# Kernel optimization log

Hardware: AMD Instinct MI355X
Metric: run time of the kernel (lower is better)

The kernel has to match this reference:

```python
import jax, jax.numpy as jnp
import numpy as np

NU = 500000   # num user nodes
NI = 100000   # num item nodes
F  = 300      # item feature dim
D  = 64       # hidden channels
E  = 2000000  # num rated edges
EL = 1000000  # num supervision (label) edges


def setup_inputs() -> dict:
    key = jax.random.key(0)
    ks = jax.random.split(key, 24)
    def nrm(k, shp, scale=0.05):
        return jax.random.normal(k, shp, dtype=jnp.float32) * scale
    inp = {
        "user_emb_w": nrm(ks[0], (NU, D)),
        "item_x": jax.random.normal(ks[1], (NI, F), dtype=jnp.float32),
        "item_lin_w": nrm(ks[2], (F, D)),
        "item_lin_b": jnp.zeros((D,), jnp.float32),
        "Wl1_ui": nrm(ks[3], (D, D)), "Wr1_ui": nrm(ks[4], (D, D)), "b1_ui": jnp.zeros((D,), jnp.float32),
        "Wl1_iu": nrm(ks[5], (D, D)), "Wr1_iu": nrm(ks[6], (D, D)), "b1_iu": jnp.zeros((D,), jnp.float32),
        "Wl2_ui": nrm(ks[7], (D, D)), "Wr2_ui": nrm(ks[8], (D, D)), "b2_ui": jnp.zeros((D,), jnp.float32),
        "Wl2_iu": nrm(ks[9], (D, D)), "Wr2_iu": nrm(ks[10], (D, D)), "b2_iu": jnp.zeros((D,), jnp.float32),
        "user_node_id": jnp.arange(NU, dtype=jnp.int32),
        "edge_src": jax.random.randint(ks[11], (E,), 0, NU, dtype=jnp.int32),
        "edge_dst": jax.random.randint(ks[12], (E,), 0, NI, dtype=jnp.int32),
        "label_src": jax.random.randint(ks[13], (EL,), 0, NU, dtype=jnp.int32),
        "label_dst": jax.random.randint(ks[14], (EL,), 0, NI, dtype=jnp.int32),
    }
    return inp


def _seg_mean(x_src, src, dst, n_dst):
    # mean-aggregate source features onto destination nodes (PyG SAGEConv aggr='mean')
    s = jax.ops.segment_sum(x_src[src], dst, num_segments=n_dst)
    c = jax.ops.segment_sum(jnp.ones(src.shape, x_src.dtype), dst, num_segments=n_dst)
    return s / jnp.maximum(c, 1.0)[:, None]


def reference(user_emb_w, item_x, item_lin_w, item_lin_b,
              Wl1_ui, Wr1_ui, b1_ui, Wl1_iu, Wr1_iu, b1_iu,
              Wl2_ui, Wr2_ui, b2_ui, Wl2_iu, Wr2_iu, b2_iu,
              user_node_id, edge_src, edge_dst, label_src, label_dst):
    # input layers: user embedding lookup, item linear projection
    x_user = user_emb_w[user_node_id]                 # [NU, D]
    x_item = item_x @ item_lin_w + item_lin_b         # [NI, D]

    def hetero_sage(xu, xi, Wl_ui, Wr_ui, bui, Wl_iu, Wr_iu, biu):
        # edge type (user, rates, item): aggregate user msgs at items
        hi = _seg_mean(xu, edge_src, edge_dst, NI) @ Wl_ui + bui + xi @ Wr_ui
        # edge type (item, rev_rates, user): aggregate item msgs at users
        hu = _seg_mean(xi, edge_dst, edge_src, NU) @ Wl_iu + biu + xu @ Wr_iu
        return hu, hi

    hu, hi = hetero_sage(x_user, x_item, Wl1_ui, Wr1_ui, b1_ui, Wl1_iu, Wr1_iu, b1_iu)
    hu, hi = jax.nn.relu(hu), jax.nn.relu(hi)
    hu, hi = hetero_sage(hu, hi, Wl2_ui, Wr2_ui, b2_ui, Wl2_iu, Wr2_iu, b2_iu)

    # DOT predictor on edge_label_index pairs
    return jnp.sum(hu[label_src] * hi[label_dst], axis=-1)   # [EL]
```

## Files before the change

kernel.cpp:

```cpp
#include <hip/hip_runtime.h>

#define NUu 500000
#define NIi 100000
#define FDIM 300
#define DDIM 64
#define NEe 2000000
#define ELl 1000000
#define EMAX (NEe - 1)

#define BSZL_I 9
#define BSZL_U 10
#define NB_I 196
#define NB_U 489
#define NBT (NB_I + NB_U)
#define SH_I 19
#define SH_U 17
#define EPB 8192
#define KPB 32

#define DBINS 64

typedef __attribute__((ext_vector_type(8))) short s8v;
typedef __attribute__((ext_vector_type(4))) short s4v;
typedef __attribute__((ext_vector_type(4))) float f4v;
typedef __attribute__((ext_vector_type(4))) unsigned u4v;
typedef unsigned short u16;

__device__ __forceinline__ float bf2f(u16 h) {
    union { unsigned u; float f; } x; x.u = ((unsigned)h) << 16; return x.f;
}
__device__ __forceinline__ u16 f2bf(float f) {
    union { float f; unsigned u; } x; x.f = f;
    unsigned u = x.u;
    u += 0x7FFFu + ((u >> 16) & 1u);
    return (u16)(u >> 16);
}
__device__ __forceinline__ float lo2f(unsigned u) {
    union { unsigned x; float f; } c; c.x = u << 16; return c.f;
}
__device__ __forceinline__ float hi2f(unsigned u) {
    union { unsigned x; float f; } c; c.x = u & 0xffff0000u; return c.f;
}

__global__ __launch_bounds__(256) void k_cast_users(const float* __restrict__ ue,
                                                    const int* __restrict__ uid,
                                                    u16* __restrict__ xu) {
    int idx = blockIdx.x * 256 + threadIdx.x;
    int n  = idx >> 4;
    int d0 = (idx & 15) * 4;
    int src = uid[n];
    const float4* p = (const float4*)(ue + (size_t)src * DDIM + d0);
    float4 v = *p;
    s4v o;
    o[0] = (short)f2bf(v.x); o[1] = (short)f2bf(v.y);
    o[2] = (short)f2bf(v.z); o[3] = (short)f2bf(v.w);
    *(s4v*)(xu + (size_t)n * DDIM + d0) = o;
}

__global__ __launch_bounds__(256) void k_cast_w(const float* __restrict__ W,
                                                u16* __restrict__ wbf) {
    int idx = blockIdx.x * 256 + threadIdx.x;
    if (idx >= 2560) return;
    int f = idx >> 6, lane = idx & 63;
    int q = lane >> 4, c = lane & 15;
    int kstep = f >> 2, nb = f & 3;
    u16* dst = wbf + (size_t)idx * 8;
#pragma unroll
    for (int j = 0; j < 8; j++) {
        int k = kstep * 32 + q * 8 + j;
        float v = (k < FDIM) ? W[k * DDIM + nb * 16 + c] : 0.f;
        dst[j] = f2bf(v);
    }
}

__global__ __launch_bounds__(256) void k_cast_w8(
    const float* __restrict__ W0, const float* __restrict__ W1,
    const float* __restrict__ W2, const float* __restrict__ W3,
    const float* __restrict__ W4, const float* __restrict__ W5,
    const float* __restrict__ W6, const float* __restrict__ W7,
    u16* __restrict__ out) {
    int idx = blockIdx.x * 256 + threadIdx.x;
    if (idx >= 4096) return;
    int wm = idx >> 9;
    int s = idx & 511;
    int ks = s >> 8, nb = (s >> 6) & 3, lane = s & 63;
    int q = lane >> 4, c = lane & 15;
    const float* W;
    switch (wm) {
        case 0: W = W0; break; case 1: W = W1; break;
        case 2: W = W2; break; case 3: W = W3; break;
        case 4: W = W4; break; case 5: W = W5; break;
        case 6: W = W6; break; default: W = W7; break;
    }
    u16* dst = out + (size_t)idx * 8;
#pragma unroll
    for (int j = 0; j < 8; j++) {
        int row = ks * 32 + q * 8 + j;
        dst[j] = f2bf(W[row * DDIM + nb * 16 + c]);
    }
}

__global__ __launch_bounds__(256) void k_item_lin2(const float* __restrict__ ix,
                                                   const u16* __restrict__ wbf,
                                                   const float* __restrict__ b,
                                                   u16* __restrict__ xi) {
    __shared__ __align__(16) u16 wl[40 * 64 * 8];
    int tid = threadIdx.x;
    for (int i = tid; i < 2560; i += 256)
        ((f4v*)wl)[i] = ((const f4v*)wbf)[i];
    __syncthreads();

    int lane = tid & 63;
    int q = lane >> 4, c = lane & 15;
    float bv[4];
#pragma unroll
    for (int nb = 0; nb < 4; nb++) bv[nb] = b[nb * 16 + c];

    int w = blockIdx.x * 4 + (tid >> 6);
    int stride = gridDim.x * 4;
    const int NT = NIi / 16;
    for (int t = w; t < NT; t += stride) {
        int row = t * 16 + c;
        const float* xr = ix + (size_t)row * FDIM;
        f4v acc[4];
#pragma unroll
        for (int nb = 0; nb < 4; nb++) {
            acc[nb][0] = bv[nb]; acc[nb][1] = bv[nb];
            acc[nb][2] = bv[nb]; acc[nb][3] = bv[nb];
        }
#pragma unroll
        for (int ks = 0; ks < 10; ks++) {
            s8v a;
            if (ks < 9 || q == 0) {
                float4 v0 = *(const float4*)(xr + ks * 32 + q * 8);
                float4 v1 = *(const float4*)(xr + ks * 32 + q * 8 + 4);
                a[0] = (short)f2bf(v0.x); a[1] = (short)f2bf(v0.y);
                a[2] = (short)f2bf(v0.z); a[3] = (short)f2bf(v0.w);
                a[4] = (short)f2bf(v1.x); a[5] = (short)f2bf(v1.y);
                a[6] = (short)f2bf(v1.z); a[7] = (short)f2bf(v1.w);
            } else {
                float4 v0 = *(const float4*)(xr + 296);
                a[0] = (short)f2bf(v0.x); a[1] = (short)f2bf(v0.y);
                a[2] = (short)f2bf(v0.z); a[3] = (short)f2bf(v0.w);
                a[4] = 0; a[5] = 0; a[6] = 0; a[7] = 0;
            }
#pragma unroll
            for (int nb = 0; nb < 4; nb++) {
                s8v bb = *(const s8v*)(wl + ((size_t)(ks * 4 + nb) * 64 + lane) * 8);
                acc[nb] = __builtin_amdgcn_mfma_f32_16x16x32_bf16(a, bb, acc[nb], 0, 0, 0);
            }
        }
#pragma unroll
        for (int nb = 0; nb < 4; nb++)
#pragma unroll
            for (int r = 0; r < 4; r++)
                xi[(size_t)(t * 16 + q * 4 + r) * DDIM + nb * 16 + c] = f2bf(acc[nb][r]);
    }
}

__global__ __launch_bounds__(256) void k_hist(const int* __restrict__ src,
                                              const int* __restrict__ dst,
                                              int* __restrict__ hist) {
    __shared__ int h[NBT];
    int t = threadIdx.x;
    for (int c = t; c < NBT; c += 256) h[c] = 0;
    __syncthreads();
    int base = blockIdx.x * EPB;
    for (int k = 0; k < KPB; k++) {
        int e = base + k * 256 + t;
        if (e < NEe) {
            int s = src[e], d = dst[e];
            atomicAdd(&h[d >> BSZL_I], 1);
            atomicAdd(&h[NB_I + (s >> BSZL_U)], 1);
        }
    }
    __syncthreads();
    for (int c = t; c < NBT; c += 256) {
        int n = h[c];
        if (n) atomicAdd(&hist[c], n);
    }
}

__device__ __forceinline__ void scanN(const int* __restrict__ cnt, int n, int total,
                                      int* __restrict__ base, int* __restrict__ frontier,
                                      int* sb) {
    int t = threadIdx.x;
    int v[8]; int s = 0;
#pragma unroll
    for (int i = 0; i < 8; i++) {
        int idx = t * 8 + i;
        v[i] = (idx < n) ? cnt[idx] : 0;
        s += v[i];
    }
    sb[t] = s; __syncthreads();
    for (int o = 1; o < 256; o <<= 1) {
        int a = (t >= o) ? sb[t - o] : 0;
        __syncthreads();
        sb[t] += a;
        __syncthreads();
    }
    int run = sb[t] - s;
#pragma unroll
    for (int i = 0; i < 8; i++) {
        int idx = t * 8 + i;
        if (idx < n) { base[idx] = run; frontier[idx] = run; }
        run += v[i];
    }
    if (t == 0) base[n] = total;
    __syncthreads();
}

__global__ __launch_bounds__(256) void k_bucket_scan(const int* __restrict__ hist,
                                                     int* __restrict__ base_i, int* __restrict__ fr_i,
                                                     int* __restrict__ base_u, int* __restrict__ fr_u,
                                                     int* __restrict__ rpi, int* __restrict__ rpu) {
    __shared__ int sb[256];
    scanN(hist, NB_I, NEe, base_i, fr_i, sb);
    scanN(hist + NB_I, NB_U, NEe, base_u, fr_u, sb);
    if (threadIdx.x == 0) { rpi[NIi] = NEe; rpu[NUu] = NEe; }
}

__global__ __launch_bounds__(256) void k_scatter(const int* __restrict__ src,
                                                 const int* __restrict__ dst,
                                                 int* __restrict__ fr_i, int* __restrict__ fr_u,
                                                 unsigned* __restrict__ scat_i,
                                                 unsigned* __restrict__ scat_u) {
    __shared__ int h[NBT];
    int t = threadIdx.x;
    for (int c = t; c < NBT; c += 256) h[c] = 0;
    __syncthreads();
    int base = blockIdx.x * EPB;
    for (int k = 0; k < KPB; k++) {
        int e = base + k * 256 + t;
        if (e < NEe) {
            int s = src[e], d = dst[e];
            atomicAdd(&h[d >> BSZL_I], 1);
            atomicAdd(&h[NB_I + (s >> BSZL_U)], 1);
        }
    }
    __syncthreads();
    for (int c = t; c < NBT; c += 256) {
        int n = h[c];
        if (n) {
            int b = (c < NB_I) ? atomicAdd(&fr_i[c], n) : atomicAdd(&fr_u[c - NB_I], n);
            h[c] = b;
        }
    }
    __syncthreads();
    for (int k = 0; k < KPB; k++) {
        int e = base + k * 256 + t;
        if (e < NEe) {
            int s = src[e], d = dst[e];
            int p = atomicAdd(&h[d >> BSZL_I], 1);
            scat_i[p] = (unsigned)s | ((unsigned)(d & ((1 << BSZL_I) - 1)) << SH_I);
            int q = atomicAdd(&h[NB_I + (s >> BSZL_U)], 1);
            scat_u[q] = (unsigned)d | ((unsigned)(s & ((1 << BSZL_U) - 1)) << SH_U);
        }
    }
}

__global__ __launch_bounds__(256) void k_bfill(const unsigned* __restrict__ scat,
                                               const int* __restrict__ base,
                                               int* __restrict__ rp, int* __restrict__ col,
                                               int shift, int bszlog, int ntotal) {
    __shared__ int cnt[1024];
    __shared__ int pos[1024];
    __shared__ int sb[256];
    int b = blockIdx.x;
    int t = threadIdx.x;
    int e0 = base[b], e1 = base[b + 1];
    int node0 = b << bszlog;
    int bsz = 1 << bszlog;
    unsigned mask = (1u << shift) - 1u;

    for (int c = t; c < bsz; c += 256) cnt[c] = 0;
    __syncthreads();
    for (int e = e0 + t; e < e1; e += 256) {
        unsigned v = scat[e];
        atomicAdd(&cnt[v >> shift], 1);
    }
    __syncthreads();
    int per = bsz >> 8;
    int loc[4]; int ls = 0;
#pragma unroll
    for (int i = 0; i < 4; i++) {
        loc[i] = (i < per) ? cnt[t * per + i] : 0;
        ls += loc[i];
    }
    sb[t] = ls; __syncthreads();
    for (int o = 1; o < 256; o <<= 1) {
        int a = (t >= o) ? sb[t - o] : 0;
        __syncthreads();
        sb[t] += a;
        __syncthreads();
    }
    int run = e0 + sb[t] - ls;
#pragma unroll
    for (int i = 0; i < 4; i++) {
        if (i < per) {
            int idx = t * per + i;
            int node = node0 + idx;
            if (node < ntotal) rp[node] = run;
            pos[idx] = run;
            run += loc[i];
        }
    }
    __syncthreads();
    for (int e = e0 + t; e < e1; e += 256) {
        unsigned v = scat[e];
        int l = v >> shift;
        int p = atomicAdd(&pos[l], 1);
        col[p] = (int)(v & mask);
    }
}

__global__ __launch_bounds__(256) void k_dhist(const int* __restrict__ rp,
                                               int* __restrict__ hist, int n) {
    __shared__ int h[DBINS];
    int t = threadIdx.x;
    if (t < DBINS) h[t] = 0;
    __syncthreads();
    int base = blockIdx.x * 2048;
#pragma unroll
    for (int k = 0; k < 8; k++) {
        int i = base + k * 256 + t;
        if (i < n) {
            int d = rp[i + 1] - rp[i];
            atomicAdd(&h[min(d, DBINS - 1)], 1);
        }
    }
    __syncthreads();
    if (t < DBINS) { int v = h[t]; if (v) atomicAdd(&hist[t], v); }
}

__global__ void k_dscan2(int* __restrict__ hu, int* __restrict__ hi) {
    int t = threadIdx.x;
    int* h = (t < 64) ? hu : hi;
    int tt = t & 63;
    int v = h[tt];
    int s = v;
#pragma unroll
    for (int o = 1; o < 64; o <<= 1) {
        int a = __shfl_up(s, o);
        if (tt >= o) s += a;
    }
    h[tt] = s - v;
}

__global__ __launch_bounds__(256) void k_dscatter(const int* __restrict__ rp,
                                                  int* __restrict__ bpos,
                                                  int* __restrict__ nsort,
                                                  int2* __restrict__ nmeta, int n) {
    __shared__ int h[DBINS];
    __shared__ int bb[DBINS];
    int t = threadIdx.x;
    if (t < DBINS) h[t] = 0;
    __syncthreads();
    int base = blockIdx.x * 2048;
    int d[8], s0[8];
#pragma unroll
    for (int k = 0; k < 8; k++) {
        int i = base + k * 256 + t;
        if (i < n) {
            int a = rp[i], b = rp[i + 1];
            s0[k] = a;
            d[k] = b - a;
            atomicAdd(&h[min(d[k], DBINS - 1)], 1);
        } else d[k] = -1;
    }
    __syncthreads();
    if (t < DBINS) {
        int v = h[t];
        bb[t] = v ? atomicAdd(&bpos[t], v) : 0;
        h[t] = 0;
    }
    __syncthreads();
#pragma unroll
    for (int k = 0; k < 8; k++) {
        if (d[k] >= 0) {
            int bin = min(d[k], DBINS - 1);
            int p = bb[bin] + atomicAdd(&h[bin], 1);
            nsort[p] = base + k * 256 + t;
            nmeta[p] = make_int2(s0[k], d[k]);
        }
    }
}

__device__ __forceinline__ void acc_pair(float m, u4v v0, u4v v1,
                                         float* A, float* B) {
#pragma unroll
    for (int k = 0; k < 4; k++) {
        A[2 * k]     = fmaf(m, lo2f(v0[k]), A[2 * k]);
        A[2 * k + 1] = fmaf(m, hi2f(v0[k]), A[2 * k + 1]);
        B[2 * k]     = fmaf(m, lo2f(v1[k]), B[2 * k]);
        B[2 * k + 1] = fmaf(m, hi2f(v1[k]), B[2 * k + 1]);
    }
}

__global__ __launch_bounds__(256) void k_fused(const u16* __restrict__ feat,
                                               const u16* __restrict__ xf,
                                               const u16* __restrict__ wfrag,
                                               const float* __restrict__ bias,
                                               u16* __restrict__ out,
                                               const int* __restrict__ nsort,
                                               const int2* __restrict__ nmeta,
                                               const int* __restrict__ col,
                                               int ntiles, int relu) {
    __shared__ __align__(16) u16 wsh[8192];
    int tid = threadIdx.x;
    for (int i = tid; i < 1024; i += 256)
        ((f4v*)wsh)[i] = ((const f4v*)wfrag)[i];
    __syncthreads();

    int lane = tid & 63;
    int q = lane >> 4, c = lane & 15;
    int w = blockIdx.x * 4 + (tid >> 6);
    int stride = gridDim.x * 4;
    float bv[4];
#pragma unroll
    for (int nb = 0; nb < 4; nb++) bv[nb] = bias[nb * 16 + c];

    for (int t = w; t < ntiles; t += stride) {
        int idx = t * 16 + c;
        int node = nsort[idx];
        int2 meta = nmeta[idx];
        int s0 = meta.x;
        int deg = meta.y;
        float inv = (deg > 0) ? 1.0f / (float)deg : 0.0f;

        const s8v* px = (const s8v*)(xf + (size_t)node * DDIM + q * 8);
        s8v x0 = px[0], x1 = px[4];

        float accA[8] = {0.f, 0.f, 0.f, 0.f, 0.f, 0.f, 0.f, 0.f};
        float accB[8] = {0.f, 0.f, 0.f, 0.f, 0.f, 0.f, 0.f, 0.f};

        for (int i = 0; __any(i < deg); i += 4) {
            int b = s0 + i;
            int e0 = min(b,     EMAX);
            int e1 = min(b + 1, EMAX);
            int e2 = min(b + 2, EMAX);
            int e3 = min(b + 3, EMAX);
            int r0 = col[e0], r1 = col[e1], r2 = col[e2], r3 = col[e3];
            float m0 = (i     < deg) ? inv : 0.f;
            float m1 = (i + 1 < deg) ? inv : 0.f;
            float m2 = (i + 2 < deg) ? inv : 0.f;
            float m3 = (i + 3 < deg) ? inv : 0.f;
            const u4v* f0 = (const u4v*)(feat + (size_t)r0 * DDIM + q * 8);
            const u4v* f1 = (const u4v*)(feat + (size_t)r1 * DDIM + q * 8);
            const u4v* f2 = (const u4v*)(feat + (size_t)r2 * DDIM + q * 8);
            const u4v* f3 = (const u4v*)(feat + (size_t)r3 * DDIM + q * 8);
            u4v a00 = f0[0], a01 = f0[4];
            u4v a10 = f1[0], a11 = f1[4];
            u4v a20 = f2[0], a21 = f2[4];
            u4v a30 = f3[0], a31 = f3[4];
            acc_pair(m0, a00, a01, accA, accB);
            acc_pair(m1, a10, a11, accA, accB);
            acc_pair(m2, a20, a21, accA, accB);
            acc_pair(m3, a30, a31, accA, accB);
        }

        s8v a0, a1;
#pragma unroll
        for (int j = 0; j < 8; j++) {
            a0[j] = (short)f2bf(accA[j]);
            a1[j] = (short)f2bf(accB[j]);
        }

        f4v acc[4];
#pragma unroll
        for (int nb = 0; nb < 4; nb++) {
            acc[nb][0] = bv[nb]; acc[nb][1] = bv[nb];
            acc[nb][2] = bv[nb]; acc[nb][3] = bv[nb];
        }

        unsigned lz = (unsigned)lane * 8u;
        asm volatile("" : "+v"(lz));
        const u16* wb = wsh + lz;
#pragma unroll
        for (int nb = 0; nb < 4; nb++) {
            s8v wl0 = *(const s8v*)(wb + nb * 512);
            s8v wl1 = *(const s8v*)(wb + 2048 + nb * 512);
            s8v wr0 = *(const s8v*)(wb + 4096 + nb * 512);
            s8v wr1 = *(const s8v*)(wb + 6144 + nb * 512);
            acc[nb] = __builtin_amdgcn_mfma_f32_16x16x32_bf16(a0, wl0, acc[nb], 0, 0, 0);
            acc[nb] = __builtin_amdgcn_mfma_f32_16x16x32_bf16(a1, wl1, acc[nb], 0, 0, 0);
            acc[nb] = __builtin_amdgcn_mfma_f32_16x16x32_bf16(x0, wr0, acc[nb], 0, 0, 0);
            acc[nb] = __builtin_amdgcn_mfma_f32_16x16x32_bf16(x1, wr1, acc[nb], 0, 0, 0);
        }

        int rn[4];
        rn[0] = __shfl(node, q * 4 + 0);
        rn[1] = __shfl(node, q * 4 + 1);
        rn[2] = __shfl(node, q * 4 + 2);
        rn[3] = __shfl(node, q * 4 + 3);
#pragma unroll
        for (int nb = 0; nb < 4; nb++)
#pragma unroll
            for (int r = 0; r < 4; r++) {
                float v = acc[nb][r];
                if (relu) v = fmaxf(v, 0.f);
                out[(size_t)rn[r] * DDIM + nb * 16 + c] = f2bf(v);
            }
    }
}

__global__ __launch_bounds__(256) void k_dot(const u16* __restrict__ hu,
                                             const u16* __restrict__ hi,
                                             const int* __restrict__ ls,
                                             const int* __restrict__ ld,
                                             float* __restrict__ out) {
    int lane = threadIdx.x & 63;
    int sub = lane >> 3, t8 = lane & 7;
    int w = blockIdx.x * 4 + (threadIdx.x >> 6);
    int stride = gridDim.x * 4;
    const int ngroups = ELl / 8;
    for (int g = w; g < ngroups; g += stride) {
        int e = g * 8 + sub;
        int u = ls[e], it = ld[e];
        s8v av = *(const s8v*)(hu + (size_t)u  * DDIM + t8 * 8);
        s8v bv = *(const s8v*)(hi + (size_t)it * DDIM + t8 * 8);
        float s = 0.f;
#pragma unroll
        for (int k = 0; k < 8; k++) s += bf2f((u16)av[k]) * bf2f((u16)bv[k]);
        s += __shfl_xor(s, 4);
        s += __shfl_xor(s, 2);
        s += __shfl_xor(s, 1);
        if (t8 == 0) out[e] = s;
    }
}

extern "C" void kernel_launch(void* const* d_in, const int* in_sizes, int n_in,
                              void* d_out, int out_size, void* d_ws, size_t ws_size,
                              hipStream_t stream) {
    const float* user_emb = (const float*)d_in[0];
    const float* item_x   = (const float*)d_in[1];
    const float* item_w   = (const float*)d_in[2];
    const float* item_b   = (const float*)d_in[3];
    const float* Wl1_ui = (const float*)d_in[4];
    const float* Wr1_ui = (const float*)d_in[5];
    const float* b1_ui  = (const float*)d_in[6];
    const float* Wl1_iu = (const float*)d_in[7];
    const float* Wr1_iu = (const float*)d_in[8];
    const float* b1_iu  = (const float*)d_in[9];
    const float* Wl2_ui = (const float*)d_in[10];
    const float* Wr2_ui = (const float*)d_in[11];
    const float* b2_ui  = (const float*)d_in[12];
    const float* Wl2_iu = (const float*)d_in[13];
    const float* Wr2_iu = (const float*)d_in[14];
    const float* b2_iu  = (const float*)d_in[15];
    const int* uid  = (const int*)d_in[16];
    const int* esrc = (const int*)d_in[17];
    const int* edst = (const int*)d_in[18];
    const int* lsrc = (const int*)d_in[19];
    const int* ldst = (const int*)d_in[20];
    float* out = (float*)d_out;

    char* ws = (char*)d_ws;
    size_t off = 0;
    auto alloc = [&](size_t bytes) -> void* {
        void* p = ws + off;
        off += (bytes + 255) & ~(size_t)255;
        return p;
    };
    u16* xu_b   = (u16*)alloc((size_t)NUu * DDIM * 2);
    u16* hu1_b  = (u16*)alloc((size_t)NUu * DDIM * 2);
    u16* hu2_b  = (u16*)alloc((size_t)NUu * DDIM * 2);
    u16* xi_b   = (u16*)alloc((size_t)NIi * DDIM * 2);
    u16* hi1_b  = (u16*)alloc((size_t)NIi * DDIM * 2);
    u16* hi2_b  = (u16*)alloc((size_t)NIi * DDIM * 2);
    int* coli = (int*)alloc((size_t)NEe * 4);
    int* colu = (int*)alloc((size_t)NEe * 4);
    int* rpi  = (int*)alloc((size_t)(NIi + 1) * 4);
    int* rpu  = (int*)alloc((size_t)(NUu + 1) * 4);
    int* hist   = (int*)alloc((size_t)NBT * 4);
    int* base_i = (int*)alloc((size_t)(NB_I + 1) * 4);
    int* base_u = (int*)alloc((size_t)(NB_U + 1) * 4);
    int* fr_i   = (int*)alloc((size_t)NB_I * 4);
    int* fr_u   = (int*)alloc((size_t)NB_U * 4);
    u16* wbf    = (u16*)alloc((size_t)40 * 64 * 8 * 2);
    u16* wfrag2 = (u16*)alloc((size_t)4 * 8192 * 2);
    int* nsort_i  = (int*)alloc((size_t)NIi * 4);
    int2* nmeta_i = (int2*)alloc((size_t)NIi * 8);
    int* nsort_u  = (int*)alloc((size_t)NUu * 4);
    int2* nmeta_u = (int2*)alloc((size_t)NUu * 8);
    int* dhist_i  = (int*)alloc((size_t)DBINS * 4);
    int* dhist_u  = (int*)alloc((size_t)DBINS * 4);
    unsigned* scat_i = (unsigned*)xu_b;
    unsigned* scat_u = (unsigned*)((char*)xu_b + (size_t)NEe * 4);

    hipMemsetAsync(hist, 0, (size_t)NBT * 4, stream);
    hipMemsetAsync(dhist_i, 0, (size_t)DBINS * 4, stream);
    hipMemsetAsync(dhist_u, 0, (size_t)DBINS * 4, stream);
    int nchunks = (NEe + EPB - 1) / EPB;
    k_hist<<<nchunks, 256, 0, stream>>>(esrc, edst, hist);
    k_bucket_scan<<<1, 256, 0, stream>>>(hist, base_i, fr_i, base_u, fr_u, rpi, rpu);
    k_scatter<<<nchunks, 256, 0, stream>>>(esrc, edst, fr_i, fr_u, scat_i, scat_u);
    k_bfill<<<NB_I, 256, 0, stream>>>(scat_i, base_i, rpi, coli, SH_I, BSZL_I, NIi);
    k_bfill<<<NB_U, 256, 0, stream>>>(scat_u, base_u, rpu, colu, SH_U, BSZL_U, NUu);

    int nci = (NIi + 2047) / 2048;
    int ncu = (NUu + 2047) / 2048;
    k_dhist<<<nci, 256, 0, stream>>>(rpi, dhist_i, NIi);
    k_dhist<<<ncu, 256, 0, stream>>>(rpu, dhist_u, NUu);
    k_dscan2<<<1, 128, 0, stream>>>(dhist_u, dhist_i);
    k_dscatter<<<nci, 256, 0, stream>>>(rpi, dhist_i, nsort_i, nmeta_i, NIi);
    k_dscatter<<<ncu, 256, 0, stream>>>(rpu, dhist_u, nsort_u, nmeta_u, NUu);

    k_cast_w<<<10, 256, 0, stream>>>(item_w, wbf);
    k_cast_w8<<<16, 256, 0, stream>>>(Wl1_ui, Wr1_ui, Wl1_iu, Wr1_iu,
                                      Wl2_ui, Wr2_ui, Wl2_iu, Wr2_iu, wfrag2);
    k_cast_users<<<NUu * 16 / 256, 256, 0, stream>>>(user_emb, uid, xu_b);
    k_item_lin2<<<1024, 256, 0, stream>>>(item_x, wbf, item_b, xi_b);

    const int NT_I = NIi / 16;
    const int NT_U = NUu / 16;

    k_fused<<<1568, 256, 0, stream>>>(xu_b, xi_b, wfrag2 + 0 * 8192, b1_ui,
                                      hi1_b, nsort_i, nmeta_i, coli, NT_I, 1);
    k_fused<<<2048, 256, 0, stream>>>(xi_b, xu_b, wfrag2 + 1 * 8192, b1_iu,
                                      hu1_b, nsort_u, nmeta_u, colu, NT_U, 1);
    k_fused<<<1568, 256, 0, stream>>>(hu1_b, hi1_b, wfrag2 + 2 * 8192, b2_ui,
                                      hi2_b, nsort_i, nmeta_i, coli, NT_I, 0);
    k_fused<<<2048, 256, 0, stream>>>(hi1_b, hu1_b, wfrag2 + 3 * 8192, b2_iu,
                                      hu2_b, nsort_u, nmeta_u, colu, NT_U, 0);

    k_dot<<<2048, 256, 0, stream>>>(hu2_b, hi2_b, lsrc, ldst, out);
}
```

Measured before the change: 773.2 us.

## Software-pipeline index loads and stage output through LDS for coalesced stores

```diff
diff --git a/kernel.cpp b/kernel.cpp
--- a/kernel.cpp
+++ b/kernel.cpp
@@ -407,6 +407,7 @@
                                                const int* __restrict__ col,
                                                int ntiles, int relu) {
     __shared__ __align__(16) u16 wsh[8192];
+    __shared__ __align__(16) u16 csh[4][16][72];
     int tid = threadIdx.x;
     for (int i = tid; i < 1024; i += 256)
         ((f4v*)wsh)[i] = ((const f4v*)wfrag)[i];
@@ -414,19 +415,33 @@
 
     int lane = tid & 63;
     int q = lane >> 4, c = lane & 15;
-    int w = blockIdx.x * 4 + (tid >> 6);
+    int wv = tid >> 6;
+    int w = blockIdx.x * 4 + wv;
     int stride = gridDim.x * 4;
     float bv[4];
 #pragma unroll
     for (int nb = 0; nb < 4; nb++) bv[nb] = bias[nb * 16 + c];
 
+    u16 (*crow)[72] = csh[wv];
+    int row0 = lane >> 3, c80 = lane & 7;
+    const int idmax = ntiles * 16 - 1;
+
+    if (w >= ntiles) return;
+
+    int idx0 = w * 16 + c;
+    int node = nsort[idx0];
+    int2 meta = nmeta[idx0];
+    int s0 = meta.x, deg = meta.y;
+    float inv = (deg > 0) ? 1.0f / (float)deg : 0.0f;
+    int cc0 = col[min(s0,     EMAX)];
+    int cc1 = col[min(s0 + 1, EMAX)];
+    int cc2 = col[min(s0 + 2, EMAX)];
+    int cc3 = col[min(s0 + 3, EMAX)];
+
     for (int t = w; t < ntiles; t += stride) {
-        int idx = t * 16 + c;
-        int node = nsort[idx];
-        int2 meta = nmeta[idx];
-        int s0 = meta.x;
-        int deg = meta.y;
-        float inv = (deg > 0) ? 1.0f / (float)deg : 0.0f;
+        int idxN = min((t + stride) * 16 + c, idmax);
+        int nodeN = nsort[idxN];
+        int2 metaN = nmeta[idxN];
 
         const s8v* px = (const s8v*)(xf + (size_t)node * DDIM + q * 8);
         s8v x0 = px[0], x1 = px[4];
@@ -434,21 +449,20 @@
         float accA[8] = {0.f, 0.f, 0.f, 0.f, 0.f, 0.f, 0.f, 0.f};
         float accB[8] = {0.f, 0.f, 0.f, 0.f, 0.f, 0.f, 0.f, 0.f};
 
-        for (int i = 0; __any(i < deg); i += 4) {
-            int b = s0 + i;
-            int e0 = min(b,     EMAX);
-            int e1 = min(b + 1, EMAX);
-            int e2 = min(b + 2, EMAX);
-            int e3 = min(b + 3, EMAX);
-            int r0 = col[e0], r1 = col[e1], r2 = col[e2], r3 = col[e3];
+        int g0 = cc0, g1 = cc1, g2 = cc2, g3 = cc3;
+        for (int i = 0; ;) {
+            int p0 = col[min(s0 + i + 4, EMAX)];
+            int p1 = col[min(s0 + i + 5, EMAX)];
+            int p2 = col[min(s0 + i + 6, EMAX)];
+            int p3 = col[min(s0 + i + 7, EMAX)];
             float m0 = (i     < deg) ? inv : 0.f;
             float m1 = (i + 1 < deg) ? inv : 0.f;
             float m2 = (i + 2 < deg) ? inv : 0.f;
             float m3 = (i + 3 < deg) ? inv : 0.f;
-            const u4v* f0 = (const u4v*)(feat + (size_t)r0 * DDIM + q * 8);
-            const u4v* f1 = (const u4v*)(feat + (size_t)r1 * DDIM + q * 8);
-            const u4v* f2 = (const u4v*)(feat + (size_t)r2 * DDIM + q * 8);
-            const u4v* f3 = (const u4v*)(feat + (size_t)r3 * DDIM + q * 8);
+            const u4v* f0 = (const u4v*)(feat + (size_t)g0 * DDIM + q * 8);
+            const u4v* f1 = (const u4v*)(feat + (size_t)g1 * DDIM + q * 8);
+            const u4v* f2 = (const u4v*)(feat + (size_t)g2 * DDIM + q * 8);
+            const u4v* f3 = (const u4v*)(feat + (size_t)g3 * DDIM + q * 8);
             u4v a00 = f0[0], a01 = f0[4];
             u4v a10 = f1[0], a11 = f1[4];
             u4v a20 = f2[0], a21 = f2[4];
@@ -457,7 +471,17 @@
             acc_pair(m1, a10, a11, accA, accB);
             acc_pair(m2, a20, a21, accA, accB);
             acc_pair(m3, a30, a31, accA, accB);
-        }
+            i += 4;
+            if (!__any(i < deg)) break;
+            g0 = p0; g1 = p1; g2 = p2; g3 = p3;
+        }
+
+        int s0N = metaN.x, degN = metaN.y;
+        float invN = (degN > 0) ? 1.0f / (float)degN : 0.0f;
+        cc0 = col[min(s0N,     EMAX)];
+        cc1 = col[min(s0N + 1, EMAX)];
+        cc2 = col[min(s0N + 2, EMAX)];
+        cc3 = col[min(s0N + 3, EMAX)];
 
         s8v a0, a1;
 #pragma unroll
@@ -488,19 +512,22 @@
             acc[nb] = __builtin_amdgcn_mfma_f32_16x16x32_bf16(x1, wr1, acc[nb], 0, 0, 0);
         }
 
-        int rn[4];
-        rn[0] = __shfl(node, q * 4 + 0);
-        rn[1] = __shfl(node, q * 4 + 1);
-        rn[2] = __shfl(node, q * 4 + 2);
-        rn[3] = __shfl(node, q * 4 + 3);
 #pragma unroll
         for (int nb = 0; nb < 4; nb++)
 #pragma unroll
             for (int r = 0; r < 4; r++) {
                 float v = acc[nb][r];
                 if (relu) v = fmaxf(v, 0.f);
-                out[(size_t)rn[r] * DDIM + nb * 16 + c] = f2bf(v);
+                crow[q * 4 + r][nb * 16 + c] = f2bf(v);
             }
+        s8v v0 = *(const s8v*)&crow[row0][c80 * 8];
+        s8v v1 = *(const s8v*)&crow[8 + row0][c80 * 8];
+        int n0 = __shfl(node, row0);
+        int n1 = __shfl(node, 8 + row0);
+        *(s8v*)(out + (size_t)n0 * DDIM + c80 * 8) = v0;
+        *(s8v*)(out + (size_t)n1 * DDIM + c80 * 8) = v1;
+
+        node = nodeN; s0 = s0N; deg = degN; inv = invN;
     }
 }
 
@@ -615,13 +642,13 @@
     const int NT_I = NIi / 16;
     const int NT_U = NUu / 16;
 
-    k_fused<<<1568, 256, 0, stream>>>(xu_b, xi_b, wfrag2 + 0 * 8192, b1_ui,
+    k_fused<<<1536, 256, 0, stream>>>(xu_b, xi_b, wfrag2 + 0 * 8192, b1_ui,
                                       hi1_b, nsort_i, nmeta_i, coli, NT_I, 1);
-    k_fused<<<2048, 256, 0, stream>>>(xi_b, xu_b, wfrag2 + 1 * 8192, b1_iu,
+    k_fused<<<1536, 256, 0, stream>>>(xi_b, xu_b, wfrag2 + 1 * 8192, b1_iu,
                                       hu1_b, nsort_u, nmeta_u, colu, NT_U, 1);
-    k_fused<<<1568, 256, 0, stream>>>(hu1_b, hi1_b, wfrag2 + 2 * 8192, b2_ui,
+    k_fused<<<1536, 256, 0, stream>>>(hu1_b, hi1_b, wfrag2 + 2 * 8192, b2_ui,
                                       hi2_b, nsort_i, nmeta_i, coli, NT_I, 0);
-    k_fused<<<2048, 256, 0, stream>>>(hi1_b, hu1_b, wfrag2 + 3 * 8192, b2_iu,
+    k_fused<<<1536, 256, 0, stream>>>(hi1_b, hu1_b, wfrag2 + 3 * 8192, b2_iu,
                                       hu2_b, nsort_u, nmeta_u, colu, NT_U, 0);
 
     k_dot<<<2048, 256, 0, stream>>>(hu2_b, hi2_b, lsrc, ldst, out);
```

After: 771.5 us. Within noise of the previous version (-0.2%).
